# Performance work log

Measured on AMD Instinct MI355X. Metric: run time of the kernel, lower is better.

Reference implementation:

```python
import jax, jax.numpy as jnp
import numpy as np

N_NODES = 100000
N_EDGES = 6400000
IN_CH = 128
HID = 32
OUT = 16


def setup_inputs() -> dict:
    key = jax.random.key(0)
    k1, k2, k3, k4 = jax.random.split(key, 4)
    x = jax.random.normal(k1, (N_NODES, IN_CH), dtype=jnp.float32)
    edge_index = jax.random.randint(k2, (2, N_EDGES), 0, N_NODES, dtype=jnp.int64)
    # Glorot-style init like PyG GCNConv
    W1 = jax.random.normal(k3, (IN_CH, HID), dtype=jnp.float32) * (1.0 / np.sqrt(IN_CH))
    b1 = jnp.zeros((HID,), dtype=jnp.float32)
    W2 = jax.random.normal(k4, (HID, OUT), dtype=jnp.float32) * (1.0 / np.sqrt(HID))
    b2 = jnp.zeros((OUT,), dtype=jnp.float32)
    return {"x": x, "edge_index": edge_index, "W1": W1, "b1": b1, "W2": W2, "b2": b2}


def _gcn_layer(h, W, b, row, col, norm, n_nodes):
    # transform then propagate (PyG GCNConv order)
    m = h @ W                                   # [N, F_out]
    msg = m[row] * norm[:, None]                # gather + scale, [E+N, F_out]
    agg = jax.ops.segment_sum(msg, col, num_segments=n_nodes)
    return agg + b


def reference(x, edge_index, W1, b1, W2, b2):
    n = x.shape[0]
    loops = jnp.arange(n, dtype=edge_index.dtype)
    row = jnp.concatenate([edge_index[0], loops])  # source
    col = jnp.concatenate([edge_index[1], loops])  # target (aggregation index)
    # symmetric GCN normalization with self-loops; deg >= 1 always
    deg = jax.ops.segment_sum(jnp.ones_like(col, dtype=x.dtype), col, num_segments=n)
    deg_inv_sqrt = jax.lax.rsqrt(deg)
    norm = deg_inv_sqrt[row] * deg_inv_sqrt[col]
    h = jax.nn.relu(_gcn_layer(x, W1, b1, row, col, norm, n))
    # dropout p=0.5 is identity in eval mode
    return _gcn_layer(h, W2, b2, row, col, norm, n)
```

## Files before the change

### kernel.cpp

```cpp
#include <hip/hip_runtime.h>
#include <hip/hip_bf16.h>

#define IN_CH 128
#define HID 32
#define OUT_CH 16
#define NPW 128
#define NPW_SHIFT 7
#define NB_MAX 1024
#define CAPF 12800
#define FBT 512
#define CAP 12288
#define KEYS (NPW * 2)
#define SCAN_CHUNK 1024
#define NXCD 8
#define EPT 8

typedef int vint4 __attribute__((ext_vector_type(4)));
typedef vint4 vint4u __attribute__((aligned(4)));
typedef float vfloat2 __attribute__((ext_vector_type(2)));

__global__ void detect_dtype(const void* ei, long long ecount, int n, int* flag) {
    int lane = threadIdx.x;
    const long long* p = (const long long*)ei;
    long long st = ecount / 64; if (st < 1) st = 1;
    long long idx = (long long)lane * st;
    bool ok = true;
    if (idx < ecount) {
        long long v = p[idx];
        ok = (v >= 0 && v < n);
    }
    unsigned long long mask = __ballot(ok);
    if (lane == 0) *flag = (mask == ~0ULL) ? 1 : 0;
}

__device__ __forceinline__ int load_idx(const void* ei, long long i, int is64) {
    return is64 ? (int)((const long long*)ei)[i] : ((const int*)ei)[i];
}

__device__ __forceinline__ void load_idx8_nt(const void* ei, long long off, int is64,
                                             int* c) {
    if (is64) {
        const long long* p = (const long long*)ei + off;
#pragma unroll
        for (int j = 0; j < 8; ++j) c[j] = (int)__builtin_nontemporal_load(p + j);
    } else {
        vint4 v0 = __builtin_nontemporal_load((const vint4*)((const int*)ei + off));
        vint4 v1 = __builtin_nontemporal_load((const vint4*)((const int*)ei + off + 4));
        c[0] = v0.x; c[1] = v0.y; c[2] = v0.z; c[3] = v0.w;
        c[4] = v1.x; c[5] = v1.y; c[6] = v1.z; c[7] = v1.w;
    }
}

__device__ __forceinline__ float bf_lo(unsigned int u) { return __uint_as_float(u << 16); }
__device__ __forceinline__ float bf_hi(unsigned int u) { return __uint_as_float(u & 0xFFFF0000u); }

__device__ __forceinline__ unsigned int pack_bf16(float a, float b) {
    __hip_bfloat16 ha = __float2bfloat16(a), hb = __float2bfloat16(b);
    unsigned short ua = *reinterpret_cast<unsigned short*>(&ha);
    unsigned short ub = *reinterpret_cast<unsigned short*>(&hb);
    return (unsigned int)ua | ((unsigned int)ub << 16);
}

__global__ __launch_bounds__(256) void zero_int(int* p, int n) {
    int i = blockIdx.x * 256 + threadIdx.x;
    if (i < n) p[i] = 0;
}

__global__ __launch_bounds__(256) void zero_float(float* p, long long n) {
    long long i = (long long)blockIdx.x * 256 + threadIdx.x;
    if (i < n) p[i] = 0.f;
}

__global__ __launch_bounds__(FBT) void bucket_hist(const void* ei, long long E,
                                                   const int* flag, int* bhist,
                                                   int nb, long long chunk, int fbgrid) {
    __shared__ int hist[NB_MAX];
    for (int i = threadIdx.x; i < nb; i += FBT) hist[i] = 0;
    __syncthreads();
    long long lo = (long long)blockIdx.x * chunk;
    long long hi = lo + chunk; if (hi > E) hi = E;
    int is64 = *flag;
    if ((E & 7) == 0) {
        for (long long e = lo + (long long)threadIdx.x * EPT; e + EPT <= hi;
             e += (long long)FBT * EPT) {
            int c[8]; load_idx8_nt(ei, E + e, is64, c);
#pragma unroll
            for (int j = 0; j < 8; ++j) atomicAdd(&hist[c[j] >> NPW_SHIFT], 1);
        }
    } else {
        for (long long e = lo + threadIdx.x; e < hi; e += FBT)
            atomicAdd(&hist[load_idx(ei, E + e, is64) >> NPW_SHIFT], 1);
    }
    __syncthreads();
    for (int b = threadIdx.x; b < nb; b += FBT)
        bhist[(long long)b * fbgrid + blockIdx.x] = hist[b];
}

__global__ __launch_bounds__(256) void scan_blocks(const int* bhist, int* bexcl,
                                                   int* btot, int nb, int fbgrid) {
    __shared__ int sd[256];
    int b = blockIdx.x, t = threadIdx.x;
    const int* p = bhist + (long long)b * fbgrid;
    int* q = bexcl + (long long)b * fbgrid;
    int running = 0;
    for (int j0 = 0; j0 < fbgrid; j0 += 256) {
        int j = j0 + t;
        int v = (j < fbgrid) ? p[j] : 0;
        sd[t] = v; __syncthreads();
        for (int off = 1; off < 256; off <<= 1) {
            int u = (t >= off) ? sd[t - off] : 0;
            __syncthreads(); sd[t] += u; __syncthreads();
        }
        if (j < fbgrid) q[j] = running + sd[t] - v;
        int tot = sd[255];
        __syncthreads();
        running += tot;
    }
    if (t == 0) btot[b] = running;
}

__global__ __launch_bounds__(1024) void scan_buckets(const int* btot, int* bstart, int nb) {
    __shared__ int sd[1024];
    int t = threadIdx.x;
    int a0 = (2 * t < nb) ? btot[2 * t] : 0;
    int a1 = (2 * t + 1 < nb) ? btot[2 * t + 1] : 0;
    sd[t] = a0 + a1; __syncthreads();
    for (int off = 1; off < 1024; off <<= 1) {
        int v = (t >= off) ? sd[t - off] : 0;
        __syncthreads(); sd[t] += v; __syncthreads();
    }
    int excl = sd[t] - (a0 + a1);
    if (2 * t < nb)     bstart[2 * t] = excl;
    if (2 * t + 1 < nb) bstart[2 * t + 1] = excl + a0;
    if (t == 1023) bstart[nb] = sd[t];
}

__global__ __launch_bounds__(FBT) void fill_sort(const void* ei, long long E,
                                                 const int* flag, const int* bhist,
                                                 const int* bexcl, const int* bstart,
                                                 int* bucketed, int nb,
                                                 long long chunk, int fbgrid) {
    __shared__ int lds[CAPF];
    __shared__ int hist[NB_MAX];
    __shared__ int base[NB_MAX];
    __shared__ int cur[NB_MAX];
    int blk = blockIdx.x, t = threadIdx.x;
    long long lo = (long long)blk * chunk;
    long long hi = lo + chunk; if (hi > E) hi = E;
    int cnt = (int)(hi - lo);
    for (int b = t; b < nb; b += FBT)
        hist[b] = bhist[(long long)b * fbgrid + blk];
    __syncthreads();
    int is64 = *flag;
    bool vec = ((E & 7) == 0) && ((chunk & 7) == 0);

    if (cnt <= CAPF) {
        int a0 = (2 * t < nb) ? hist[2 * t] : 0;
        int a1 = (2 * t + 1 < nb) ? hist[2 * t + 1] : 0;
        base[t] = a0 + a1; __syncthreads();
        for (int off = 1; off < FBT; off <<= 1) {
            int u = (t >= off) ? base[t - off] : 0;
            __syncthreads(); base[t] += u; __syncthreads();
        }
        int incl = base[t];
        __syncthreads();
        int excl = incl - (a0 + a1);
        if (2 * t < nb)     { base[2 * t] = excl;          cur[2 * t] = excl; }
        if (2 * t + 1 < nb) { base[2 * t + 1] = excl + a0; cur[2 * t + 1] = excl + a0; }
        __syncthreads();

        if (vec) {
            for (long long e = lo + (long long)t * EPT; e + EPT <= hi; e += (long long)FBT * EPT) {
                int c[8], r[8];
                load_idx8_nt(ei, E + e, is64, c);
                load_idx8_nt(ei, e, is64, r);
#pragma unroll
                for (int j = 0; j < 8; ++j) {
                    int b = c[j] >> NPW_SHIFT;
                    int p = atomicAdd(&cur[b], 1);
                    lds[p] = r[j] | ((c[j] & (NPW - 1)) << 17);
                }
            }
        } else {
            for (long long e = lo + t; e < hi; e += FBT) {
                int col = load_idx(ei, E + e, is64);
                int row = load_idx(ei, e, is64);
                int b = col >> NPW_SHIFT;
                int p = atomicAdd(&cur[b], 1);
                lds[p] = row | ((col & (NPW - 1)) << 17);
            }
        }
        __syncthreads();

        int grp = t >> 4, lane = t & 15;
        for (int b = grp; b < nb; b += 32) {
            int l0 = base[b], c0 = hist[b];
            if (!c0) continue;
            int g0 = bstart[b] + bexcl[(long long)b * fbgrid + blk];
            for (int j = lane; j < c0; j += 16)
                bucketed[g0 + j] = lds[l0 + j];
        }
    } else {
        for (int b = t; b < nb; b += FBT)
            cur[b] = bstart[b] + bexcl[(long long)b * fbgrid + blk];
        __syncthreads();
        for (long long e = lo + t; e < hi; e += FBT) {
            int col = load_idx(ei, E + e, is64);
            int row = load_idx(ei, e, is64);
            int b = col >> NPW_SHIFT;
            int p = atomicAdd(&cur[b], 1);
            bucketed[p] = row | ((col & (NPW - 1)) << 17);
        }
    }
}

__global__ __launch_bounds__(512) void csr_sort(const int* __restrict__ bucketed,
                                                const int* __restrict__ bstart,
                                                int* __restrict__ csr,
                                                int* __restrict__ offs,
                                                int* __restrict__ mid,
                                                float* __restrict__ dinv,
                                                int nb, int n, int nhalf) {
    __shared__ int lds_e[CAP];
    __shared__ int histk[KEYS];
    __shared__ int cur[KEYS];
    int b = blockIdx.x, t = threadIdx.x;
    int s0 = bstart[b], s1 = bstart[b + 1];
    int cnt = s1 - s0;
    if (t < KEYS) histk[t] = 0;
    __syncthreads();
    bool fit = (cnt <= CAP);
    int cnt4 = cnt & ~3;
    auto key = [&](int e) {
        return (((e >> 17) & (NPW - 1)) << 1) | (((e & 0x1FFFF) >= nhalf) ? 1 : 0);
    };
    if (fit) {
        for (int i = t * 4; i < cnt4; i += 2048) {
            vint4u e4 = *(const vint4u*)(bucketed + s0 + i);
            lds_e[i + 0] = e4.x; atomicAdd(&histk[key(e4.x)], 1);
            lds_e[i + 1] = e4.y; atomicAdd(&histk[key(e4.y)], 1);
            lds_e[i + 2] = e4.z; atomicAdd(&histk[key(e4.z)], 1);
            lds_e[i + 3] = e4.w; atomicAdd(&histk[key(e4.w)], 1);
        }
        for (int i = cnt4 + t; i < cnt; i += 512) {
            int e = bucketed[s0 + i];
            lds_e[i] = e;
            atomicAdd(&histk[key(e)], 1);
        }
    } else {
        for (int i = t * 4; i < cnt4; i += 2048) {
            vint4u e4 = *(const vint4u*)(bucketed + s0 + i);
            atomicAdd(&histk[key(e4.x)], 1);
            atomicAdd(&histk[key(e4.y)], 1);
            atomicAdd(&histk[key(e4.z)], 1);
            atomicAdd(&histk[key(e4.w)], 1);
        }
        for (int i = cnt4 + t; i < cnt; i += 512)
            atomicAdd(&histk[key(bucketed[s0 + i])], 1);
    }
    __syncthreads();
    if (t == 0) {
        int run = 0;
        for (int k = 0; k < KEYS; ++k) { cur[k] = run; run += histk[k]; }
    }
    __syncthreads();
    if (t < NPW) {
        int node = b * NPW + t;
        if (node < n) {
            offs[node] = s0 + cur[2 * t];
            mid[node]  = s0 + cur[2 * t] + histk[2 * t];
            dinv[node] = 1.0f / sqrtf((float)(histk[2 * t] + histk[2 * t + 1] + 1));
        }
    }
    if (b == nb - 1 && t == 0) offs[n] = s1;
    __syncthreads();
    if (fit) {
        for (int i = t; i < cnt; i += 512) {
            int e = lds_e[i];
            int pos = atomicAdd(&cur[key(e)], 1);
            csr[s0 + pos] = e & 0x1FFFF;
        }
    } else {
        for (int i = t; i < cnt; i += 512) {
            int e = bucketed[s0 + i];
            int pos = atomicAdd(&cur[key(e)], 1);
            csr[s0 + pos] = e & 0x1FFFF;
        }
    }
}

__global__ __launch_bounds__(256) void gemm1q(const float* __restrict__ x,
                                              const float* __restrict__ W1,
                                              const float* __restrict__ dinv,
                                              unsigned int* __restrict__ m1b, int n) {
    long long node = (long long)blockIdx.x * 256 + threadIdx.x;
    if (node >= n) return;
    const int cb = blockIdx.y * 8;
    float acc[8];
#pragma unroll
    for (int c = 0; c < 8; ++c) acc[c] = 0.f;
    const float4* xr = (const float4*)(x + node * IN_CH);
    for (int k4 = 0; k4 < IN_CH / 4; ++k4) {
        float4 xv = xr[k4];
        const float* w0 = W1 + (k4 * 4) * HID + cb;
#pragma unroll
        for (int c = 0; c < 8; ++c) acc[c] = fmaf(xv.x, w0[c], acc[c]);
#pragma unroll
        for (int c = 0; c < 8; ++c) acc[c] = fmaf(xv.y, w0[HID + c], acc[c]);
#pragma unroll
        for (int c = 0; c < 8; ++c) acc[c] = fmaf(xv.z, w0[2 * HID + c], acc[c]);
#pragma unroll
        for (int c = 0; c < 8; ++c) acc[c] = fmaf(xv.w, w0[3 * HID + c], acc[c]);
    }
    float di = dinv[node];
    unsigned int* dst = m1b + (node << 4) + blockIdx.y * 4;
#pragma unroll
    for (int c = 0; c < 4; ++c)
        dst[c] = pack_bf16(acc[2 * c] * di, acc[2 * c + 1] * di);
}

__global__ __launch_bounds__(256) void gemm2q(const float* __restrict__ h,
                                              const float* __restrict__ W2,
                                              const float* __restrict__ dinv,
                                              unsigned int* __restrict__ m2b, int n) {
    long long node = (long long)blockIdx.x * 256 + threadIdx.x;
    if (node >= n) return;
    const int cb = blockIdx.y * 8;
    float acc[8];
#pragma unroll
    for (int c = 0; c < 8; ++c) acc[c] = 0.f;
    const float4* hr = (const float4*)(h + (node << 5));
    for (int k4 = 0; k4 < HID / 4; ++k4) {
        float4 hv = hr[k4];
        const float* w0 = W2 + (k4 * 4) * OUT_CH + cb;
#pragma unroll
        for (int c = 0; c < 8; ++c) acc[c] = fmaf(hv.x, w0[c], acc[c]);
#pragma unroll
        for (int c = 0; c < 8; ++c) acc[c] = fmaf(hv.y, w0[OUT_CH + c], acc[c]);
#pragma unroll
        for (int c = 0; c < 8; ++c) acc[c] = fmaf(hv.z, w0[2 * OUT_CH + c], acc[c]);
#pragma unroll
        for (int c = 0; c < 8; ++c) acc[c] = fmaf(hv.w, w0[3 * OUT_CH + c], acc[c]);
    }
    float di = dinv[node];
    unsigned int* dst = m2b + (node << 3) + blockIdx.y * 4;
#pragma unroll
    for (int c = 0; c < 4; ++c)
        dst[c] = pack_bf16(acc[2 * c] * di, acc[2 * c + 1] * di);
}

__global__ __launch_bounds__(256) void gemm1f(const float* __restrict__ x,
                                              const float* __restrict__ W1,
                                              const float* __restrict__ dinv,
                                              float* __restrict__ m1f, int n) {
    long long node = (long long)blockIdx.x * 256 + threadIdx.x;
    if (node >= n) return;
    float acc[HID];
#pragma unroll
    for (int c = 0; c < HID; ++c) acc[c] = 0.f;
    const float4* xr = (const float4*)(x + node * IN_CH);
    for (int k4 = 0; k4 < IN_CH / 4; ++k4) {
        float4 xv = xr[k4];
        const float* w0 = W1 + (k4 * 4) * HID;
#pragma unroll
        for (int c = 0; c < HID; ++c) acc[c] = fmaf(xv.x, w0[c], acc[c]);
#pragma unroll
        for (int c = 0; c < HID; ++c) acc[c] = fmaf(xv.y, w0[HID + c], acc[c]);
#pragma unroll
        for (int c = 0; c < HID; ++c) acc[c] = fmaf(xv.z, w0[2 * HID + c], acc[c]);
#pragma unroll
        for (int c = 0; c < HID; ++c) acc[c] = fmaf(xv.w, w0[3 * HID + c], acc[c]);
    }
    float di = dinv[node];
    float4* dst = (float4*)(m1f + (node << 5));
#pragma unroll
    for (int c = 0; c < HID / 4; ++c) {
        float4 v;
        v.x = acc[4 * c] * di;     v.y = acc[4 * c + 1] * di;
        v.z = acc[4 * c + 2] * di; v.w = acc[4 * c + 3] * di;
        dst[c] = v;
    }
}

__global__ __launch_bounds__(256) void gemm2f(const float* __restrict__ h,
                                              const float* __restrict__ W2,
                                              const float* __restrict__ dinv,
                                              float* __restrict__ m2f, int n) {
    long long node = (long long)blockIdx.x * 256 + threadIdx.x;
    if (node >= n) return;
    float acc[OUT_CH];
#pragma unroll
    for (int c = 0; c < OUT_CH; ++c) acc[c] = 0.f;
    const float4* hr = (const float4*)(h + (node << 5));
    for (int k4 = 0; k4 < HID / 4; ++k4) {
        float4 hv = hr[k4];
        const float* w0 = W2 + (k4 * 4) * OUT_CH;
#pragma unroll
        for (int c = 0; c < OUT_CH; ++c) acc[c] = fmaf(hv.x, w0[c], acc[c]);
#pragma unroll
        for (int c = 0; c < OUT_CH; ++c) acc[c] = fmaf(hv.y, w0[OUT_CH + c], acc[c]);
#pragma unroll
        for (int c = 0; c < OUT_CH; ++c) acc[c] = fmaf(hv.z, w0[2 * OUT_CH + c], acc[c]);
#pragma unroll
        for (int c = 0; c < OUT_CH; ++c) acc[c] = fmaf(hv.w, w0[3 * OUT_CH + c], acc[c]);
    }
    float di = dinv[node];
    float4* dst = (float4*)(m2f + (node << 4));
#pragma unroll
    for (int c = 0; c < OUT_CH / 4; ++c) {
        float4 v;
        v.x = acc[4 * c] * di;     v.y = acc[4 * c + 1] * di;
        v.z = acc[4 * c + 2] * di; v.w = acc[4 * c + 3] * di;
        dst[c] = v;
    }
}

template <int MODE>
__global__ __launch_bounds__(256) void agg1_bf(const unsigned int* __restrict__ m1b,
                                               const int* __restrict__ csr,
                                               const int* __restrict__ offs,
                                               const int* __restrict__ mid,
                                               const float* __restrict__ dinv,
                                               const float* __restrict__ b1,
                                               float* __restrict__ h, int n) {
    int g = threadIdx.x >> 4;
    int c = threadIdx.x & 15;
    long long node = (long long)blockIdx.x * 16 + g;
    if (node >= n) return;
    int s, e1;
    if (MODE == 0)      { s = offs[node]; e1 = mid[node]; }
    else if (MODE == 1) { s = mid[node];  e1 = offs[node + 1]; }
    else                { s = offs[node]; e1 = offs[node + 1]; }
    float accL, accH;
    if (MODE == 0) { accL = 0.f; accH = 0.f; }
    else {
        unsigned int us = m1b[(node << 4) + c];
        accL = bf_lo(us); accH = bf_hi(us);
    }
    for (; s + 7 < e1; s += 8) {
        vint4u a = *(const vint4u*)(csr + s);
        vint4u b = *(const vint4u*)(csr + s + 4);
        unsigned int u0 = m1b[((long long)a.x << 4) + c];
        unsigned int u1 = m1b[((long long)a.y << 4) + c];
        unsigned int u2 = m1b[((long long)a.z << 4) + c];
        unsigned int u3 = m1b[((long long)a.w << 4) + c];
        unsigned int u4 = m1b[((long long)b.x << 4) + c];
        unsigned int u5 = m1b[((long long)b.y << 4) + c];
        unsigned int u6 = m1b[((long long)b.z << 4) + c];
        unsigned int u7 = m1b[((long long)b.w << 4) + c];
        accL += bf_lo(u0); accH += bf_hi(u0);
        accL += bf_lo(u1); accH += bf_hi(u1);
        accL += bf_lo(u2); accH += bf_hi(u2);
        accL += bf_lo(u3); accH += bf_hi(u3);
        accL += bf_lo(u4); accH += bf_hi(u4);
        accL += bf_lo(u5); accH += bf_hi(u5);
        accL += bf_lo(u6); accH += bf_hi(u6);
        accL += bf_lo(u7); accH += bf_hi(u7);
    }
    for (; s < e1; ++s) {
        unsigned int u = m1b[((long long)csr[s] << 4) + c];
        accL += bf_lo(u); accH += bf_hi(u);
    }
    if (MODE == 0) {
        vfloat2 val; val.x = accL; val.y = accH;
        __builtin_nontemporal_store(val, (vfloat2*)(h + (node << 5) + 2 * c));
    } else {
        if (MODE == 1) {
            vfloat2 prev = __builtin_nontemporal_load((const vfloat2*)(h + (node << 5) + 2 * c));
            accL += prev.x; accH += prev.y;
        }
        float di = dinv[node];
        float vL = accL * di + b1[2 * c];
        float vH = accH * di + b1[2 * c + 1];
        vfloat2 val;
        val.x = vL > 0.f ? vL : 0.f;
        val.y = vH > 0.f ? vH : 0.f;
        *(vfloat2*)(h + (node << 5) + 2 * c) = val;
    }
}

__global__ __launch_bounds__(256) void agg2_bf(const unsigned int* __restrict__ m2b,
                                               const int* __restrict__ csr,
                                               const int* __restrict__ offs,
                                               const float* __restrict__ dinv,
                                               const float* __restrict__ b2,
                                               float* __restrict__ out, int n) {
    int g = threadIdx.x >> 3;
    int c = threadIdx.x & 7;
    long long node = (long long)blockIdx.x * 32 + g;
    if (node >= n) return;
    unsigned int us = m2b[(node << 3) + c];
    float accL = bf_lo(us), accH = bf_hi(us);
    int s = offs[node], e1 = offs[node + 1];
    for (; s + 7 < e1; s += 8) {
        vint4u a = *(const vint4u*)(csr + s);
        vint4u b = *(const vint4u*)(csr + s + 4);
        unsigned int u0 = m2b[((long long)a.x << 3) + c];
        unsigned int u1 = m2b[((long long)a.y << 3) + c];
        unsigned int u2 = m2b[((long long)a.z << 3) + c];
        unsigned int u3 = m2b[((long long)a.w << 3) + c];
        unsigned int u4 = m2b[((long long)b.x << 3) + c];
        unsigned int u5 = m2b[((long long)b.y << 3) + c];
        unsigned int u6 = m2b[((long long)b.z << 3) + c];
        unsigned int u7 = m2b[((long long)b.w << 3) + c];
        accL += bf_lo(u0); accH += bf_hi(u0);
        accL += bf_lo(u1); accH += bf_hi(u1);
        accL += bf_lo(u2); accH += bf_hi(u2);
        accL += bf_lo(u3); accH += bf_hi(u3);
        accL += bf_lo(u4); accH += bf_hi(u4);
        accL += bf_lo(u5); accH += bf_hi(u5);
        accL += bf_lo(u6); accH += bf_hi(u6);
        accL += bf_lo(u7); accH += bf_hi(u7);
    }
    for (; s < e1; ++s) {
        unsigned int u = m2b[((long long)csr[s] << 3) + c];
        accL += bf_lo(u); accH += bf_hi(u);
    }
    float di = dinv[node];
    vfloat2 val;
    val.x = accL * di + b2[2 * c];
    val.y = accH * di + b2[2 * c + 1];
    *(vfloat2*)(out + (node << 4) + 2 * c) = val;
}

__global__ __launch_bounds__(256) void count_edges(const void* ei, int* cnt,
                                                   long long E, const int* flag) {
    long long e0 = ((long long)blockIdx.x * 256 + threadIdx.x) * EPT;
    if (e0 >= E) return;
    int is64 = *flag;
    if (e0 + EPT <= E && (E & 7) == 0) {
        int c[EPT];
        load_idx8_nt(ei, E + e0, is64, c);
#pragma unroll
        for (int j = 0; j < EPT; ++j) atomicAdd(&cnt[c[j]], 1);
    } else {
        for (long long e = e0; e < E && e < e0 + EPT; ++e)
            atomicAdd(&cnt[load_idx(ei, E + e, is64)], 1);
    }
}

__global__ __launch_bounds__(256) void compute_dinv(const int* cnt, float* dinv, int n) {
    int i = blockIdx.x * 256 + threadIdx.x;
    if (i < n) dinv[i] = 1.0f / sqrtf((float)(cnt[i] + 1));
}

__global__ __launch_bounds__(256) void scan_partial(const int* cnt, int* partial, int n) {
    __shared__ int sd[256];
    int base = blockIdx.x * SCAN_CHUNK;
    int s = 0;
    for (int j = threadIdx.x; j < SCAN_CHUNK; j += 256) {
        int i = base + j;
        if (i < n) s += cnt[i];
    }
    sd[threadIdx.x] = s;
    __syncthreads();
    for (int off = 128; off > 0; off >>= 1) {
        if (threadIdx.x < off) sd[threadIdx.x] += sd[threadIdx.x + off];
        __syncthreads();
    }
    if (threadIdx.x == 0) partial[blockIdx.x] = sd[0];
}

__global__ void scan_serial(int* partial, int* offs, int nblk, int n) {
    if (threadIdx.x == 0 && blockIdx.x == 0) {
        int run = 0;
        for (int b = 0; b < nblk; ++b) { int t = partial[b]; partial[b] = run; run += t; }
        offs[n] = run;
    }
}

__global__ __launch_bounds__(256) void scan_final(const int* cnt, const int* partial,
                                                  int* offs, int n) {
    __shared__ int sd[256];
    int base = blockIdx.x * SCAN_CHUNK;
    int t = threadIdx.x;
    int loc[4]; int ts = 0;
#pragma unroll
    for (int j = 0; j < 4; ++j) {
        int i = base + t * 4 + j;
        loc[j] = (i < n) ? cnt[i] : 0;
        ts += loc[j];
    }
    sd[t] = ts;
    __syncthreads();
    for (int off = 1; off < 256; off <<= 1) {
        int v = (t >= off) ? sd[t - off] : 0;
        __syncthreads();
        sd[t] += v;
        __syncthreads();
    }
    int excl = sd[t] - ts + partial[blockIdx.x];
#pragma unroll
    for (int j = 0; j < 4; ++j) {
        int i = base + t * 4 + j;
        if (i < n) offs[i] = excl;
        excl += loc[j];
    }
}

__global__ __launch_bounds__(256) void copy_int(const int* src, int* dst, int n) {
    int i = blockIdx.x * 256 + threadIdx.x;
    if (i < n) dst[i] = src[i];
}

__global__ __launch_bounds__(256) void fill_csr_win(const void* ei, int* cursor, int* csr,
                                                    long long E, const int* flag,
                                                    int npw, int n) {
    int w = blockIdx.x & (NXCD - 1);
    int b = blockIdx.x >> 3;
    int lo = w * npw;
    int hi = lo + npw; if (hi > n) hi = n;
    long long e0 = ((long long)b * 256 + threadIdx.x) * EPT;
    if (e0 >= E) return;
    int is64 = *flag;
    if (e0 + EPT <= E && (E & 7) == 0) {
        int c[EPT];
        load_idx8_nt(ei, E + e0, is64, c);
#pragma unroll
        for (int j = 0; j < EPT; ++j) {
            if (c[j] >= lo && c[j] < hi) {
                int row = load_idx(ei, e0 + j, is64);
                int pos = atomicAdd(&cursor[c[j]], 1);
                csr[pos] = row;
            }
        }
    } else {
        for (long long e = e0; e < E && e < e0 + EPT; ++e) {
            int col = load_idx(ei, E + e, is64);
            if (col >= lo && col < hi) {
                int row = load_idx(ei, e, is64);
                int pos = atomicAdd(&cursor[col], 1);
                csr[pos] = row;
            }
        }
    }
}

__global__ __launch_bounds__(256) void scatter1(const float* __restrict__ m1s,
                                                const void* ei,
                                                float* __restrict__ h,
                                                long long E, const int* flag) {
    long long e = (long long)blockIdx.x * 8 + (threadIdx.x >> 5);
    int c = threadIdx.x & 31;
    if (e >= E) return;
    int is64 = *flag;
    int row = load_idx(ei, e, is64);
    int col = load_idx(ei, E + e, is64);
    atomicAdd(&h[(long long)col * HID + c], m1s[(long long)row * HID + c]);
}

__global__ __launch_bounds__(256) void fixup1(const float* __restrict__ m1s,
                                              const float* __restrict__ dinv,
                                              const float* __restrict__ b1,
                                              float* __restrict__ h, int n) {
    long long t = (long long)blockIdx.x * 256 + threadIdx.x;
    long long node = t >> 5; int c = (int)(t & 31);
    if (node >= n) return;
    float v = (h[node * HID + c] + m1s[node * HID + c]) * dinv[node] + b1[c];
    h[node * HID + c] = v > 0.f ? v : 0.f;
}

__global__ __launch_bounds__(256) void scatter2(const float* __restrict__ m2s,
                                                const void* ei,
                                                float* __restrict__ out,
                                                long long E, const int* flag) {
    long long e = (long long)blockIdx.x * 16 + (threadIdx.x >> 4);
    int c = threadIdx.x & 15;
    if (e >= E) return;
    int is64 = *flag;
    int row = load_idx(ei, e, is64);
    int col = load_idx(ei, E + e, is64);
    atomicAdd(&out[(long long)col * OUT_CH + c], m2s[(long long)row * OUT_CH + c]);
}

__global__ __launch_bounds__(256) void fixup2(const float* __restrict__ m2s,
                                              const float* __restrict__ dinv,
                                              const float* __restrict__ b2,
                                              float* __restrict__ out, int n) {
    long long t = (long long)blockIdx.x * 256 + threadIdx.x;
    long long node = t >> 4; int c = (int)(t & 15);
    if (node >= n) return;
    out[node * OUT_CH + c] = (out[node * OUT_CH + c] + m2s[node * OUT_CH + c]) * dinv[node] + b2[c];
}

extern "C" void kernel_launch(void* const* d_in, const int* in_sizes, int n_in,
                              void* d_out, int out_size, void* d_ws, size_t ws_size,
                              hipStream_t stream) {
    const float* x  = (const float*)d_in[0];
    const void*  ei = d_in[1];
    const float* W1 = (const float*)d_in[2];
    const float* b1 = (const float*)d_in[3];
    const float* W2 = (const float*)d_in[4];
    const float* b2 = (const float*)d_in[5];
    float* out = (float*)d_out;

    const int n = in_sizes[0] / IN_CH;
    const long long E = in_sizes[1] / 2;
    const int nb = (n + NPW - 1) / NPW;
    const int nhalf = (n + 1) / 2;

    const long long chunkF = (((E + 511) / 512) + 7) & ~7LL;
    const int fbgrid = (int)((E + chunkF - 1) / chunkF);

    char* w = (char*)d_ws;
    size_t used = 0;
    auto carve = [&](size_t bytes) -> void* {
        void* p = (void*)(w + used);
        used += (bytes + 255) & ~(size_t)255;
        return p;
    };
    auto A = [](size_t b) -> size_t { return (b + 255) & ~(size_t)255; };

    int*   bstart  = (int*)carve((size_t)(NB_MAX + 1) * 4);
    int*   btot    = (int*)carve((size_t)NB_MAX * 4);
    float* dinv    = (float*)carve((size_t)n * 4);
    int*   flag    = (int*)carve(256);
    int*   offs    = (int*)carve((size_t)(n + 1) * 4);
    int*   mid     = (int*)carve((size_t)n * 4);
    int*   cnt     = (int*)carve((size_t)n * 4);
    int*   partial = (int*)carve(4096);
    const size_t base = used;

    const size_t bhistB = A((size_t)nb * fbgrid * 4);
    const size_t mbB    = A((size_t)n * HID * 2);
    const size_t hB     = A((size_t)n * HID * 4);
    const size_t needT1 = base + 2 * bhistB + 2 * A((size_t)E * 4) + mbB + hB;
    const size_t needT2 = base + A((size_t)E * 4) + mbB + hB;
    const size_t needT3 = base + 2 * A((size_t)n * HID * 4);
    const bool tier1 = (ws_size >= needT1) && (n <= 131071) && (nb <= NB_MAX);
    const bool tier2 = !tier1 && (ws_size >= needT2) && (n <= 131071);

    const int nblkN  = (n + 255) / 256;
    const int nblkEv = (int)((E + 256LL * EPT - 1) / (256LL * EPT));
    const int nblkSc = (n + SCAN_CHUNK - 1) / SCAN_CHUNK;
    const int nblkH  = (int)(((long long)n * HID + 255) / 256);
    const int nblkO  = (int)(((long long)n * OUT_CH + 255) / 256);

    detect_dtype<<<1, 64, 0, stream>>>(ei, E, n, flag);

    if (tier1) {
        int*   bhist    = (int*)carve((size_t)nb * fbgrid * 4);
        int*   bexcl    = (int*)carve((size_t)nb * fbgrid * 4);
        int*   bucketed = (int*)carve((size_t)E * 4);
        int*   csr      = (int*)carve((size_t)E * 4);
        __hip_bfloat16* m1b = (__hip_bfloat16*)carve((size_t)n * HID * 2);
        float* h  = (float*)carve((size_t)n * HID * 4);
        __hip_bfloat16* m2b = m1b;

        bucket_hist<<<fbgrid, FBT, 0, stream>>>(ei, E, flag, bhist, nb, chunkF, fbgrid);
        scan_blocks<<<nb, 256, 0, stream>>>(bhist, bexcl, btot, nb, fbgrid);
        scan_buckets<<<1, 1024, 0, stream>>>(btot, bstart, nb);
        fill_sort<<<fbgrid, FBT, 0, stream>>>(ei, E, flag, bhist, bexcl, bstart,
                                              bucketed, nb, chunkF, fbgrid);
        csr_sort<<<nb, 512, 0, stream>>>(bucketed, bstart, csr, offs, mid, dinv,
                                         nb, n, nhalf);

        gemm1q<<<dim3(nblkN, 4), 256, 0, stream>>>(x, W1, dinv, (unsigned int*)m1b, n);
        agg1_bf<0><<<(n + 15) / 16, 256, 0, stream>>>((const unsigned int*)m1b, csr,
                                                      offs, mid, dinv, b1, h, n);
        agg1_bf<1><<<(n + 15) / 16, 256, 0, stream>>>((const unsigned int*)m1b, csr,
                                                      offs, mid, dinv, b1, h, n);
        gemm2q<<<dim3(nblkN, 2), 256, 0, stream>>>(h, W2, dinv, (unsigned int*)m2b, n);
        agg2_bf<<<(n + 31) / 32, 256, 0, stream>>>((const unsigned int*)m2b, csr, offs,
                                                   dinv, b2, out, n);
    } else if (tier2) {
        int*   csr = (int*)carve((size_t)E * 4);
        __hip_bfloat16* m1b = (__hip_bfloat16*)carve((size_t)n * HID * 2);
        float* h  = (float*)carve((size_t)n * HID * 4);
        __hip_bfloat16* m2b = m1b;

        zero_int<<<nblkN, 256, 0, stream>>>(cnt, n);
        count_edges<<<nblkEv, 256, 0, stream>>>(ei, cnt, E, flag);
        compute_dinv<<<nblkN, 256, 0, stream>>>(cnt, dinv, n);
        scan_partial<<<nblkSc, 256, 0, stream>>>(cnt, partial, n);
        scan_serial<<<1, 64, 0, stream>>>(partial, offs, nblkSc, n);
        scan_final<<<nblkSc, 256, 0, stream>>>(cnt, partial, offs, n);
        copy_int<<<nblkN, 256, 0, stream>>>(offs, cnt, n);

        const int npw2 = (n + NXCD - 1) / NXCD;
        fill_csr_win<<<nblkEv * NXCD, 256, 0, stream>>>(ei, cnt, csr, E, flag, npw2, n);

        gemm1q<<<dim3(nblkN, 4), 256, 0, stream>>>(x, W1, dinv, (unsigned int*)m1b, n);
        agg1_bf<2><<<(n + 15) / 16, 256, 0, stream>>>((const unsigned int*)m1b, csr,
                                                      offs, offs, dinv, b1, h, n);
        gemm2q<<<dim3(nblkN, 2), 256, 0, stream>>>(h, W2, dinv, (unsigned int*)m2b, n);
        agg2_bf<<<(n + 31) / 32, 256, 0, stream>>>((const unsigned int*)m2b, csr, offs,
                                                   dinv, b2, out, n);
    } else if (ws_size >= needT3) {
        float* m1 = (float*)carve((size_t)n * HID * 4);
        float* h  = (float*)carve((size_t)n * HID * 4);
        float* m2 = m1;

        zero_int<<<nblkN, 256, 0, stream>>>(cnt, n);
        count_edges<<<nblkEv, 256, 0, stream>>>(ei, cnt, E, flag);
        compute_dinv<<<nblkN, 256, 0, stream>>>(cnt, dinv, n);

        gemm1f<<<nblkN, 256, 0, stream>>>(x, W1, dinv, m1, n);
        zero_float<<<nblkH, 256, 0, stream>>>(h, (long long)n * HID);
        scatter1<<<(int)((E + 7) / 8), 256, 0, stream>>>(m1, ei, h, E, flag);
        fixup1<<<nblkH, 256, 0, stream>>>(m1, dinv, b1, h, n);
        gemm2f<<<nblkN, 256, 0, stream>>>(h, W2, dinv, m2, n);
        zero_float<<<nblkO, 256, 0, stream>>>(out, (long long)n * OUT_CH);
        scatter2<<<(int)((E + 15) / 16), 256, 0, stream>>>(m2, ei, out, E, flag);
        fixup2<<<nblkO, 256, 0, stream>>>(m2, dinv, b2, out, n);
    }
}
```

Baseline: 275.2 us.

## Split GEMM K-dimension across wavefronts with LDS reduction instead of column split

Replaces the column-split dense transforms, where each node's input row was re-read by 4 (or 2) separate blocks, with a K-split. Each wavefront computes all output channels over a quarter (or half) of the input dimension. Partial sums are then reduced through padded shared memory before the scaled bf16 pack. This removes the redundant global reads of x and h, at the cost of more accumulator registers, LDS traffic and a block barrier.

```diff
diff --git a/kernel.cpp b/kernel.cpp
--- a/kernel.cpp
+++ b/kernel.cpp
@@ -289,64 +289,98 @@
     }
 }
 
-__global__ __launch_bounds__(256) void gemm1q(const float* __restrict__ x,
+__global__ __launch_bounds__(256) void gemm1s(const float* __restrict__ x,
                                               const float* __restrict__ W1,
                                               const float* __restrict__ dinv,
                                               unsigned int* __restrict__ m1b, int n) {
-    long long node = (long long)blockIdx.x * 256 + threadIdx.x;
-    if (node >= n) return;
-    const int cb = blockIdx.y * 8;
-    float acc[8];
-#pragma unroll
-    for (int c = 0; c < 8; ++c) acc[c] = 0.f;
-    const float4* xr = (const float4*)(x + node * IN_CH);
-    for (int k4 = 0; k4 < IN_CH / 4; ++k4) {
-        float4 xv = xr[k4];
-        const float* w0 = W1 + (k4 * 4) * HID + cb;
-#pragma unroll
-        for (int c = 0; c < 8; ++c) acc[c] = fmaf(xv.x, w0[c], acc[c]);
-#pragma unroll
-        for (int c = 0; c < 8; ++c) acc[c] = fmaf(xv.y, w0[HID + c], acc[c]);
-#pragma unroll
-        for (int c = 0; c < 8; ++c) acc[c] = fmaf(xv.z, w0[2 * HID + c], acc[c]);
-#pragma unroll
-        for (int c = 0; c < 8; ++c) acc[c] = fmaf(xv.w, w0[3 * HID + c], acc[c]);
-    }
-    float di = dinv[node];
-    unsigned int* dst = m1b + (node << 4) + blockIdx.y * 4;
-#pragma unroll
-    for (int c = 0; c < 4; ++c)
-        dst[c] = pack_bf16(acc[2 * c] * di, acc[2 * c + 1] * di);
-}
-
-__global__ __launch_bounds__(256) void gemm2q(const float* __restrict__ h,
+    __shared__ float red[4 * 64 * 33];
+    int t = threadIdx.x;
+    int lane = t & 63, w = t >> 6;
+    long long node = (long long)blockIdx.x * 64 + lane;
+    float acc[HID];
+#pragma unroll
+    for (int c = 0; c < HID; ++c) acc[c] = 0.f;
+    if (node < n) {
+        const float4* xr = (const float4*)(x + node * IN_CH + w * 32);
+#pragma unroll
+        for (int j = 0; j < 8; ++j) {
+            float4 xv = xr[j];
+            const float* w0 = W1 + (w * 32 + j * 4) * HID;
+#pragma unroll
+            for (int c = 0; c < HID; ++c) acc[c] = fmaf(xv.x, w0[c], acc[c]);
+#pragma unroll
+            for (int c = 0; c < HID; ++c) acc[c] = fmaf(xv.y, w0[HID + c], acc[c]);
+#pragma unroll
+            for (int c = 0; c < HID; ++c) acc[c] = fmaf(xv.z, w0[2 * HID + c], acc[c]);
+#pragma unroll
+            for (int c = 0; c < HID; ++c) acc[c] = fmaf(xv.w, w0[3 * HID + c], acc[c]);
+        }
+    }
+    float* dst = red + (w * 64 + lane) * 33;
+#pragma unroll
+    for (int c = 0; c < HID; ++c) dst[c] = acc[c];
+    __syncthreads();
+    int nl = t & 63, cg = t >> 6;
+    long long nodeR = (long long)blockIdx.x * 64 + nl;
+    if (nodeR >= n) return;
+    float di = dinv[nodeR];
+    unsigned int* dstg = m1b + (nodeR << 4) + cg * 4;
+#pragma unroll
+    for (int p = 0; p < 4; ++p) {
+        int c0 = cg * 8 + 2 * p;
+        float s0 = red[(0 * 64 + nl) * 33 + c0] + red[(1 * 64 + nl) * 33 + c0] +
+                   red[(2 * 64 + nl) * 33 + c0] + red[(3 * 64 + nl) * 33 + c0];
+        float s1 = red[(0 * 64 + nl) * 33 + c0 + 1] + red[(1 * 64 + nl) * 33 + c0 + 1] +
+                   red[(2 * 64 + nl) * 33 + c0 + 1] + red[(3 * 64 + nl) * 33 + c0 + 1];
+        dstg[p] = pack_bf16(s0 * di, s1 * di);
+    }
+}
+
+__global__ __launch_bounds__(256) void gemm2s(const float* __restrict__ h,
                                               const float* __restrict__ W2,
                                               const float* __restrict__ dinv,
                                               unsigned int* __restrict__ m2b, int n) {
-    long long node = (long long)blockIdx.x * 256 + threadIdx.x;
-    if (node >= n) return;
-    const int cb = blockIdx.y * 8;
-    float acc[8];
-#pragma unroll
-    for (int c = 0; c < 8; ++c) acc[c] = 0.f;
-    const float4* hr = (const float4*)(h + (node << 5));
-    for (int k4 = 0; k4 < HID / 4; ++k4) {
-        float4 hv = hr[k4];
-        const float* w0 = W2 + (k4 * 4) * OUT_CH + cb;
-#pragma unroll
-        for (int c = 0; c < 8; ++c) acc[c] = fmaf(hv.x, w0[c], acc[c]);
-#pragma unroll
-        for (int c = 0; c < 8; ++c) acc[c] = fmaf(hv.y, w0[OUT_CH + c], acc[c]);
-#pragma unroll
-        for (int c = 0; c < 8; ++c) acc[c] = fmaf(hv.z, w0[2 * OUT_CH + c], acc[c]);
-#pragma unroll
-        for (int c = 0; c < 8; ++c) acc[c] = fmaf(hv.w, w0[3 * OUT_CH + c], acc[c]);
-    }
-    float di = dinv[node];
-    unsigned int* dst = m2b + (node << 3) + blockIdx.y * 4;
-#pragma unroll
-    for (int c = 0; c < 4; ++c)
-        dst[c] = pack_bf16(acc[2 * c] * di, acc[2 * c + 1] * di);
+    __shared__ float red[2 * 128 * 17];
+    int t = threadIdx.x;
+    int lane = t & 63, w = t >> 6;
+    int kh = w & 1, ng = w >> 1;
+    int nl = ng * 64 + lane;
+    long long node = (long long)blockIdx.x * 128 + nl;
+    float acc[OUT_CH];
+#pragma unroll
+    for (int c = 0; c < OUT_CH; ++c) acc[c] = 0.f;
+    if (node < n) {
+        const float4* hr = (const float4*)(h + (node << 5) + kh * 16);
+#pragma unroll
+        for (int j = 0; j < 4; ++j) {
+            float4 hv = hr[j];
+            const float* w0 = W2 + (kh * 16 + j * 4) * OUT_CH;
+#pragma unroll
+            for (int c = 0; c < OUT_CH; ++c) acc[c] = fmaf(hv.x, w0[c], acc[c]);
+#pragma unroll
+            for (int c = 0; c < OUT_CH; ++c) acc[c] = fmaf(hv.y, w0[OUT_CH + c], acc[c]);
+#pragma unroll
+            for (int c = 0; c < OUT_CH; ++c) acc[c] = fmaf(hv.z, w0[2 * OUT_CH + c], acc[c]);
+#pragma unroll
+            for (int c = 0; c < OUT_CH; ++c) acc[c] = fmaf(hv.w, w0[3 * OUT_CH + c], acc[c]);
+        }
+    }
+    float* dst = red + (kh * 128 + nl) * 17;
+#pragma unroll
+    for (int c = 0; c < OUT_CH; ++c) dst[c] = acc[c];
+    __syncthreads();
+    int nl2 = t & 127, cg = t >> 7;
+    long long nodeR = (long long)blockIdx.x * 128 + nl2;
+    if (nodeR >= n) return;
+    float di = dinv[nodeR];
+    unsigned int* dstg = m2b + (nodeR << 3) + cg * 4;
+#pragma unroll
+    for (int p = 0; p < 4; ++p) {
+        int c0 = cg * 8 + 2 * p;
+        float s0 = red[(0 * 128 + nl2) * 17 + c0] + red[(1 * 128 + nl2) * 17 + c0];
+        float s1 = red[(0 * 128 + nl2) * 17 + c0 + 1] + red[(1 * 128 + nl2) * 17 + c0 + 1];
+        dstg[p] = pack_bf16(s0 * di, s1 * di);
+    }
 }
 
 __global__ __launch_bounds__(256) void gemm1f(const float* __restrict__ x,
@@ -735,6 +769,8 @@
     const int nblkSc = (n + SCAN_CHUNK - 1) / SCAN_CHUNK;
     const int nblkH  = (int)(((long long)n * HID + 255) / 256);
     const int nblkO  = (int)(((long long)n * OUT_CH + 255) / 256);
+    const int nblkG1 = (n + 63) / 64;
+    const int nblkG2 = (n + 127) / 128;
 
     detect_dtype<<<1, 64, 0, stream>>>(ei, E, n, flag);
 
@@ -755,12 +791,12 @@
         csr_sort<<<nb, 512, 0, stream>>>(bucketed, bstart, csr, offs, mid, dinv,
                                          nb, n, nhalf);
 
-        gemm1q<<<dim3(nblkN, 4), 256, 0, stream>>>(x, W1, dinv, (unsigned int*)m1b, n);
+        gemm1s<<<nblkG1, 256, 0, stream>>>(x, W1, dinv, (unsigned int*)m1b, n);
         agg1_bf<0><<<(n + 15) / 16, 256, 0, stream>>>((const unsigned int*)m1b, csr,
                                                       offs, mid, dinv, b1, h, n);
         agg1_bf<1><<<(n + 15) / 16, 256, 0, stream>>>((const unsigned int*)m1b, csr,
                                                       offs, mid, dinv, b1, h, n);
-        gemm2q<<<dim3(nblkN, 2), 256, 0, stream>>>(h, W2, dinv, (unsigned int*)m2b, n);
+        gemm2s<<<nblkG2, 256, 0, stream>>>(h, W2, dinv, (unsigned int*)m2b, n);
         agg2_bf<<<(n + 31) / 32, 256, 0, stream>>>((const unsigned int*)m2b, csr, offs,
                                                    dinv, b2, out, n);
     } else if (tier2) {
@@ -780,10 +816,10 @@
         const int npw2 = (n + NXCD - 1) / NXCD;
         fill_csr_win<<<nblkEv * NXCD, 256, 0, stream>>>(ei, cnt, csr, E, flag, npw2, n);
 
-        gemm1q<<<dim3(nblkN, 4), 256, 0, stream>>>(x, W1, dinv, (unsigned int*)m1b, n);
+        gemm1s<<<nblkG1, 256, 0, stream>>>(x, W1, dinv, (unsigned int*)m1b, n);
         agg1_bf<2><<<(n + 15) / 16, 256, 0, stream>>>((const unsigned int*)m1b, csr,
                                                       offs, offs, dinv, b1, h, n);
-        gemm2q<<<dim3(nblkN, 2), 256, 0, stream>>>(h, W2, dinv, (unsigned int*)m2b, n);
+        gemm2s<<<nblkG2, 256, 0, stream>>>(h, W2, dinv, (unsigned int*)m2b, n);
         agg2_bf<<<(n + 31) / 32, 256, 0, stream>>>((const unsigned int*)m2b, csr, offs,
                                                    dinv, b2, out, n);
     } else if (ws_size >= needT3) {
```

New measurement: 289.7 us. +5.3%, slower.
